# Optimization experiments

Measured on AMD Instinct MI355X. Metric: run time of the kernel, lower is better.

Reference implementation:

```python
import jax, jax.numpy as jnp
import numpy as np

D_MODEL = 1024
N_HEADS = 16
HEAD_DIM = D_MODEL // N_HEADS
NEG = -10000.0  # module uses -10000, not -inf


def setup_inputs() -> dict:
    key = jax.random.key(0)
    ks = jax.random.split(key, 8)
    B, T = 4, 2048
    q = jax.random.normal(ks[0], (B, T, D_MODEL), dtype=jnp.float32)
    k = jax.random.normal(ks[1], (B, T, D_MODEL), dtype=jnp.float32)
    v = jax.random.normal(ks[2], (B, T, D_MODEL), dtype=jnp.float32)
    attn_mask = jnp.ones((B, T), dtype=jnp.float32)
    # xavier_uniform for square [d, d] weights: limit = sqrt(6/(d+d))
    lim = float(np.sqrt(6.0 / (D_MODEL + D_MODEL)))
    Wq = jax.random.uniform(ks[3], (D_MODEL, D_MODEL), jnp.float32, -lim, lim)
    Wk = jax.random.uniform(ks[4], (D_MODEL, D_MODEL), jnp.float32, -lim, lim)
    Wv = jax.random.uniform(ks[5], (D_MODEL, D_MODEL), jnp.float32, -lim, lim)
    Wo = jax.random.uniform(ks[6], (D_MODEL, D_MODEL), jnp.float32, -lim, lim)
    return {"q": q, "k": k, "v": v, "attn_mask": attn_mask,
            "Wq": Wq, "Wk": Wk, "Wv": Wv, "Wo": Wo, "mask_future": 1}


def _split_heads(x):
    B, T, _ = x.shape
    return x.reshape(B, T, N_HEADS, HEAD_DIM).transpose(0, 2, 1, 3)  # [B,H,T,D]


def reference(q, k, v, attn_mask, Wq, Wk, Wv, Wo, mask_future):
    # torch Linear: y = x @ W.T  (weights stored [out, in])
    qh = _split_heads(jnp.einsum('btd,ed->bte', q, Wq))
    kh = _split_heads(jnp.einsum('btd,ed->bte', k, Wk))
    vh = _split_heads(jnp.einsum('btd,ed->bte', v, Wv))
    L, S = qh.shape[-2], kh.shape[-2]
    # dual scale: each of q and k scaled by 1/d**0.25
    scale = 1.0 / jnp.sqrt(jnp.sqrt(jnp.float32(HEAD_DIM)))
    scores = jnp.einsum('bhld,bhsd->bhls', qh * scale, kh * scale)
    if mask_future:
        causal_bias = jnp.triu(jnp.full((L, S), NEG, dtype=scores.dtype), k=1)
        scores = scores + causal_bias
    # padding mask: attn_mask [B, S] -> broadcast [B,1,1,S]; 0 entries -> -10000
    pad = attn_mask[:, None, None, :]
    scores = jnp.where(pad == 0, jnp.asarray(NEG, scores.dtype), scores)
    probs = jax.nn.softmax(scores, axis=-1)  # dropout p=0.0 -> identity
    ctx = jnp.einsum('bhls,bhsd->bhld', probs, vh)
    B = ctx.shape[0]
    ctx = ctx.transpose(0, 2, 1, 3).reshape(B, L, D_MODEL)
    return jnp.einsum('btd,ed->bte', ctx, Wo)
```

## Files before the change

kernel.cpp:

```cpp
#include <hip/hip_runtime.h>

typedef unsigned short u16;
typedef __attribute__((ext_vector_type(8))) _Float16 f16x8;
typedef __attribute__((ext_vector_type(2))) __fp16 fp16v2;
typedef __attribute__((ext_vector_type(4))) float f32x4;
typedef __attribute__((ext_vector_type(16))) float f32x16;

#define T_SEQ 2048
#define NH 16
#define DH 64
#define DM 1024
#define NEG2 (-14426.95f)
#define QS2 (0.42466089f)

__device__ __forceinline__ unsigned pk2(float a, float b) {
  union { fp16v2 v; unsigned u; } c;
  c.v = __builtin_amdgcn_cvt_pkrtz(a, b);
  return c.u;
}
__device__ __forceinline__ u16 f2h(float a) {
  union { _Float16 h; u16 u; } c; c.h = (_Float16)a; return c.u;
}

__device__ __forceinline__ void async_load16(const void* g, void* l) {
  __builtin_amdgcn_global_load_lds(
      (const __attribute__((address_space(1))) unsigned int*)(g),
      (__attribute__((address_space(3))) unsigned int*)(l), 16, 0, 0);
}

__global__ __launch_bounds__(256) void convert_all(
    const float* __restrict__ q, const float* __restrict__ k, const float* __restrict__ v,
    const float* __restrict__ Wq, const float* __restrict__ Wk, const float* __restrict__ Wv,
    const float* __restrict__ Wo, u16* __restrict__ xb, u16* __restrict__ wb) {
  int blk = blockIdx.x;
  const float* src; u16* dst;
  if (blk < 12288) {
    int s = blk >> 12;
    src = (s == 0) ? q : (s == 1) ? k : v;
    dst = xb + (size_t)s * 8388608u;
    blk &= 4095;
  } else {
    int s = (blk - 12288) >> 9;
    src = (s == 0) ? Wq : (s == 1) ? Wk : (s == 2) ? Wv : Wo;
    dst = wb + (size_t)s * 1048576u;
    blk = (blk - 12288) & 511;
  }
  size_t base = (size_t)blk * 2048 + (size_t)threadIdx.x * 8;
  float4 a = *(const float4*)(src + base);
  float4 b2 = *(const float4*)(src + base + 4);
  uint4 st;
  st.x = pk2(a.x, a.y); st.y = pk2(a.z, a.w);
  st.z = pk2(b2.x, b2.y); st.w = pk2(b2.z, b2.w);
  *(uint4*)(dst + base) = st;
}

__global__ __launch_bounds__(256) void gemm_qkv(const u16* __restrict__ A,
                                                const u16* __restrict__ Wqb,
                                                const u16* __restrict__ Wkb,
                                                const u16* __restrict__ Wvb,
                                                u16* __restrict__ Qh, u16* __restrict__ Kh,
                                                u16* __restrict__ VTh) {
  __shared__ char lds[33792];
  const int tid = threadIdx.x;
  const int wid = tid >> 6, lane = tid & 63;
  const int l32 = lane & 31, lh = lane >> 5;
  const int m0 = blockIdx.x * 128;
  const int n0 = blockIdx.y * 128;
  const int which = n0 >> 10;
  const int n0l = n0 & 1023;
  const u16* As = A + (size_t)which * 8388608u;
  const u16* Bw = (which == 0) ? Wqb : (which == 1) ? Wkb : Wvb;
  const int wm = wid >> 1, wn = wid & 1;
  char* const rbase = (which < 2) ? (lds + 16384) : lds;
  char* const cbase = (which < 2) ? lds : (lds + 16384);
  f32x16 acc[2][2] = {};

  for (int kt = 0; kt < 1024; kt += 64) {
    __syncthreads();
    for (int i = 0; i < 4; ++i) {
      int p = wid * 4 + i;
      int mt = p >> 2, ks = p & 3;
      int col = kt + ks * 16 + lh * 8;
      async_load16(As + (size_t)(m0 + mt * 32 + l32) * 1024 + col, lds + p * 1024);
      async_load16(Bw + (size_t)(n0l + mt * 32 + l32) * 1024 + col, lds + 16384 + p * 1024);
    }
    __syncthreads();
    for (int ks = 0; ks < 4; ++ks) {
      f16x8 rf[2], cf[2];
      for (int i = 0; i < 2; ++i) {
        rf[i] = *(const f16x8*)(rbase + ((wm * 2 + i) * 4 + ks) * 1024 + lane * 16);
        cf[i] = *(const f16x8*)(cbase + ((wn * 2 + i) * 4 + ks) * 1024 + lane * 16);
      }
      for (int i = 0; i < 2; ++i)
        for (int j = 0; j < 2; ++j)
          acc[i][j] = __builtin_amdgcn_mfma_f32_32x32x16_f16(rf[i], cf[j], acc[i][j], 0, 0, 0);
    }
  }

  const float s = (which < 2) ? QS2 : 1.0f;
  __syncthreads();
  for (int i = 0; i < 2; ++i)
    for (int j = 0; j < 2; ++j) {
      int colb = wn * 64 + j * 32 + l32;
      int rowb = wm * 64 + i * 32 + 4 * lh;
      for (int g = 0; g < 4; ++g) {
        uint2 pv;
        pv.x = pk2(acc[i][j][4 * g + 0] * s, acc[i][j][4 * g + 1] * s);
        pv.y = pk2(acc[i][j][4 * g + 2] * s, acc[i][j][4 * g + 3] * s);
        *(uint2*)(lds + colb * 264 + (rowb + 8 * g) * 2) = pv;
      }
    }
  __syncthreads();

  const int b = m0 >> 11, t0 = m0 & 2047, h0 = n0l >> 6;
  if (which < 2) {
    u16* O = which ? Kh : Qh;
    for (int p = 0; p < 8; ++p) {
      int row = p * 16 + (tid >> 4);
      int seg = tid & 15;
      uint4 val = *(const uint4*)(lds + row * 264 + seg * 16);
      int hl = seg >> 3, dh0 = (seg & 7) * 8;
      *(uint4*)(O + (((size_t)(b * NH + h0 + hl) * T_SEQ + t0 + row) << 6) + dh0) = val;
    }
  } else {
    for (int p = 0; p < 8; ++p) {
      int row = p * 16 + (tid >> 4);
      int seg = tid & 15;
      uint4 val = *(const uint4*)(lds + row * 264 + seg * 16);
      int h = h0 + (row >> 6), dh = row & 63;
      *(uint4*)(VTh + (((size_t)(b * NH + h) * DH + dh) << 11) + t0 + seg * 8) = val;
    }
  }
}

__global__ __launch_bounds__(256) void gemm_out(const u16* __restrict__ A,
                                                const u16* __restrict__ Bw,
                                                float* __restrict__ O) {
  __shared__ char lds[32768];
  const int tid = threadIdx.x;
  const int wid = tid >> 6, lane = tid & 63;
  const int l32 = lane & 31, lh = lane >> 5;
  const int m0 = blockIdx.x * 128, n0 = blockIdx.y * 128;
  const int wm = wid >> 1, wn = wid & 1;
  f32x16 acc[2][2] = {};

  for (int kt = 0; kt < 1024; kt += 64) {
    __syncthreads();
    for (int i = 0; i < 4; ++i) {
      int p = wid * 4 + i;
      int mt = p >> 2, ks = p & 3;
      int col = kt + ks * 16 + lh * 8;
      async_load16(A + (size_t)(m0 + mt * 32 + l32) * 1024 + col, lds + p * 1024);
      async_load16(Bw + (size_t)(n0 + mt * 32 + l32) * 1024 + col, lds + 16384 + p * 1024);
    }
    __syncthreads();
    for (int ks = 0; ks < 4; ++ks) {
      f16x8 af[2], bf[2];
      for (int i = 0; i < 2; ++i) {
        af[i] = *(const f16x8*)(lds + ((wm * 2 + i) * 4 + ks) * 1024 + lane * 16);
        bf[i] = *(const f16x8*)(lds + 16384 + ((wn * 2 + i) * 4 + ks) * 1024 + lane * 16);
      }
      for (int i = 0; i < 2; ++i)
        for (int j = 0; j < 2; ++j)
          acc[i][j] = __builtin_amdgcn_mfma_f32_32x32x16_f16(af[i], bf[j], acc[i][j], 0, 0, 0);
    }
  }
  for (int i = 0; i < 2; ++i)
    for (int j = 0; j < 2; ++j) {
      int col = n0 + wn * 64 + j * 32 + l32;
      int rowb = m0 + wm * 64 + i * 32 + 4 * lh;
      for (int g = 0; g < 4; ++g)
        for (int rr = 0; rr < 4; ++rr)
          O[(size_t)(rowb + 8 * g + rr) * 1024 + col] = acc[i][j][4 * g + rr];
    }
}

__global__ __launch_bounds__(512) void attn_kernel(const u16* __restrict__ Qh,
                                                   const u16* __restrict__ Kh,
                                                   const u16* __restrict__ VTh,
                                                   const float* __restrict__ attn_mask,
                                                   const int* __restrict__ mfp,
                                                   u16* __restrict__ ctx) {
  __shared__ char kls[8192];
  __shared__ char vls[8192];
  __shared__ char pls[8][2048];
  __shared__ float maskb[T_SEQ];
  __shared__ int mzf;

  const int tid = threadIdx.x;
  const int wid = tid >> 6, lane = tid & 63;
  const int lm = lane & 15, lq = lane >> 4;
  const int bid = blockIdx.x;
  const int bh_i = bid & 63, p8 = bid >> 6;
  const int b = bh_i >> 4, h = bh_i & 15;
  const int mf = *mfp;
  const size_t bh = (size_t)(b * NH + h);
  const u16* Qbh = Qh + bh * T_SEQ * DH;
  const u16* Kbh = Kh + bh * T_SEQ * DH;
  const u16* VTbh = VTh + bh * DH * T_SEQ;

  if (tid == 0) mzf = 0;
  __syncthreads();
  {
    int az = 0;
    for (int i = tid; i < T_SEQ; i += 512) {
      float mv = attn_mask[(size_t)b * T_SEQ + i];
      maskb[i] = (mv == 0.0f) ? NEG2 : 0.0f;
      az |= (mv == 0.0f);
    }
    if (az) mzf = 1;
  }
  __syncthreads();
  const int maskzero = mzf;

  for (int half = 0; half < 2; ++half) {
    const int qt = half ? (15 - p8) : p8;
    const int q0 = qt * 128;
    const int qw = q0 + wid * 16;
    f16x8 qf[2];
    qf[0] = *(const f16x8*)(Qbh + (size_t)(qw + lm) * DH + lq * 8);
    qf[1] = *(const f16x8*)(Qbh + (size_t)(qw + lm) * DH + 32 + lq * 8);

    f32x4 acc[4] = {};
    float mprev = -1e30f, lsum = 0.f;

    const int nch = mf ? (qt + 1) * 2 : 32;
    for (int c = 0; c < nch; ++c) {
      const int s0 = c * 64;
      __syncthreads();
      async_load16(Kbh + (size_t)(s0 + (wid >> 1) * 16 + lm) * DH + (wid & 1) * 32 + lq * 8,
                   kls + wid * 1024);
      async_load16(VTbh + (size_t)((wid >> 1) * 16 + lm) * T_SEQ + s0 + (wid & 1) * 32 + lq * 8,
                   vls + wid * 1024);
      __syncthreads();

      f32x4 sc[4];
      for (int st = 0; st < 4; ++st) {
        f32x4 z = {0.f, 0.f, 0.f, 0.f};
        sc[st] = z;
        for (int kk = 0; kk < 2; ++kk) {
          f16x8 kf = *(const f16x8*)(kls + ((st * 2 + kk) * 64 + lane) * 16);
          sc[st] = __builtin_amdgcn_mfma_f32_16x16x32_f16(kf, qf[kk], sc[st], 0, 0, 0);
        }
      }
      if (maskzero) {
        for (int st = 0; st < 4; ++st) {
          f32x4 mb = *(const f32x4*)(maskb + s0 + st * 16 + lq * 4);
          for (int r = 0; r < 4; ++r) sc[st][r] += mb[r];
        }
      }
      if (mf && (s0 + 64 > qw)) {
        int qg = qw + lm;
        for (int st = 0; st < 4; ++st)
          for (int r = 0; r < 4; ++r)
            if (s0 + st * 16 + lq * 4 + r > qg) sc[st][r] = NEG2;
      }
      float mx = fmaxf(fmaxf(sc[0][0], sc[0][1]), fmaxf(sc[0][2], sc[0][3]));
      for (int st = 1; st < 4; ++st) {
        float t2 = fmaxf(fmaxf(sc[st][0], sc[st][1]), fmaxf(sc[st][2], sc[st][3]));
        mx = fmaxf(mx, t2);
      }
      mx = fmaxf(mx, __shfl_xor(mx, 16));
      mx = fmaxf(mx, __shfl_xor(mx, 32));
      float mn = mprev;
      if (__ballot(mx > mprev) != 0ull) {
        mn = fmaxf(mprev, mx);
        float alpha = exp2f(mprev - mn);
        for (int r = 0; r < 4; ++r) {
          float ar = __shfl(alpha, lq * 4 + r);
          for (int nt = 0; nt < 4; ++nt) acc[nt][r] *= ar;
        }
        lsum *= alpha;
        mprev = mn;
      }
      float ps = 0.f;
      for (int st = 0; st < 4; ++st)
        for (int r = 0; r < 4; ++r) {
          float p = exp2f(sc[st][r] - mn);
          sc[st][r] = p;
          ps += p;
        }
      ps += __shfl_xor(ps, 16);
      ps += __shfl_xor(ps, 32);
      lsum += ps;
      {
        char* pw = pls[wid];
        for (int st = 0; st < 4; ++st) {
          int kk = st >> 1;
          int lqp = (st & 1) * 2 + (lq >> 1);
          uint2 pv;
          pv.x = pk2(sc[st][0], sc[st][1]);
          pv.y = pk2(sc[st][2], sc[st][3]);
          *(uint2*)(pw + kk * 1024 + (lqp * 16 + lm) * 16 + (lq & 1) * 8) = pv;
        }
      }
      asm volatile("s_waitcnt lgkmcnt(0)" ::: "memory");
      for (int kk = 0; kk < 2; ++kk) {
        f16x8 pf = *(const f16x8*)(pls[wid] + kk * 1024 + lane * 16);
        for (int nt = 0; nt < 4; ++nt) {
          f16x8 vf = *(const f16x8*)(vls + ((nt * 2 + kk) * 64 + lane) * 16);
          acc[nt] = __builtin_amdgcn_mfma_f32_16x16x32_f16(pf, vf, acc[nt], 0, 0, 0);
        }
      }
    }
    float inv = 1.0f / lsum;
    for (int r = 0; r < 4; ++r) {
      float ir = __shfl(inv, lq * 4 + r);
      int t = qw + lq * 4 + r;
      for (int nt = 0; nt < 4; ++nt)
        ctx[((size_t)(b * T_SEQ + t) * DM) + h * DH + nt * 16 + lm] = f2h(acc[nt][r] * ir);
    }
  }
}

extern "C" void kernel_launch(void* const* d_in, const int* in_sizes, int n_in,
                              void* d_out, int out_size, void* d_ws, size_t ws_size,
                              hipStream_t stream) {
  const float* q = (const float*)d_in[0];
  const float* k = (const float*)d_in[1];
  const float* v = (const float*)d_in[2];
  const float* attn_mask = (const float*)d_in[3];
  const float* Wq = (const float*)d_in[4];
  const float* Wk = (const float*)d_in[5];
  const float* Wv = (const float*)d_in[6];
  const float* Wo = (const float*)d_in[7];
  const int* mf = (const int*)d_in[8];

  u16* ws = (u16*)d_ws;
  u16* qb  = ws;
  u16* wqb = ws + 3u * 8388608u;
  u16* wkb = wqb + 1048576u;
  u16* wvb = wkb + 1048576u;
  u16* wob = wvb + 1048576u;
  u16* Qh  = wob + 1048576u;
  u16* Kh  = Qh + 8388608u;
  u16* VTh = Kh + 8388608u;
  u16* ctxb = ws;

  convert_all<<<14336, 256, 0, stream>>>(q, k, v, Wq, Wk, Wv, Wo, qb, wqb);

  dim3 gq(64, 24);
  gemm_qkv<<<gq, 256, 0, stream>>>(qb, wqb, wkb, wvb, Qh, Kh, VTh);

  attn_kernel<<<512, 512, 0, stream>>>(Qh, Kh, VTh, attn_mask, mf, ctxb);

  dim3 gg(64, 8);
  gemm_out<<<gg, 256, 0, stream>>>(ctxb, wob, (float*)d_out);
}
```

Measured before the change: 382.3 us.

## Double-buffer LDS tiles in QKV and output GEMMs with prefetch

```diff
diff --git a/kernel.cpp b/kernel.cpp
--- a/kernel.cpp
+++ b/kernel.cpp
@@ -71,25 +71,33 @@
   const u16* As = A + (size_t)which * 8388608u;
   const u16* Bw = (which == 0) ? Wqb : (which == 1) ? Wkb : Wvb;
   const int wm = wid >> 1, wn = wid & 1;
-  char* const rbase = (which < 2) ? (lds + 16384) : lds;
-  char* const cbase = (which < 2) ? lds : (lds + 16384);
   f32x16 acc[2][2] = {};
 
-  for (int kt = 0; kt < 1024; kt += 64) {
+  const u16* gA = As + (size_t)(m0 + wid * 32 + l32) * 1024 + lh * 8;
+  const u16* gB = Bw + (size_t)(n0l + wid * 32 + l32) * 1024 + lh * 8;
+  async_load16(gA, lds + (wid * 2 + 0) * 1024);
+  async_load16(gA + 16, lds + (wid * 2 + 1) * 1024);
+  async_load16(gB, lds + 8192 + (wid * 2 + 0) * 1024);
+  async_load16(gB + 16, lds + 8192 + (wid * 2 + 1) * 1024);
+
+  for (int it = 0; it < 32; ++it) {
     __syncthreads();
-    for (int i = 0; i < 4; ++i) {
-      int p = wid * 4 + i;
-      int mt = p >> 2, ks = p & 3;
-      int col = kt + ks * 16 + lh * 8;
-      async_load16(As + (size_t)(m0 + mt * 32 + l32) * 1024 + col, lds + p * 1024);
-      async_load16(Bw + (size_t)(n0l + mt * 32 + l32) * 1024 + col, lds + 16384 + p * 1024);
-    }
-    __syncthreads();
-    for (int ks = 0; ks < 4; ++ks) {
+    char* cur = lds + (it & 1) * 16384;
+    if (it < 31) {
+      char* nxt = lds + ((it + 1) & 1) * 16384;
+      int kt = (it + 1) * 32;
+      async_load16(gA + kt, nxt + (wid * 2 + 0) * 1024);
+      async_load16(gA + kt + 16, nxt + (wid * 2 + 1) * 1024);
+      async_load16(gB + kt, nxt + 8192 + (wid * 2 + 0) * 1024);
+      async_load16(gB + kt + 16, nxt + 8192 + (wid * 2 + 1) * 1024);
+    }
+    char* const rb = (which < 2) ? (cur + 8192) : cur;
+    char* const cb = (which < 2) ? cur : (cur + 8192);
+    for (int ks = 0; ks < 2; ++ks) {
       f16x8 rf[2], cf[2];
       for (int i = 0; i < 2; ++i) {
-        rf[i] = *(const f16x8*)(rbase + ((wm * 2 + i) * 4 + ks) * 1024 + lane * 16);
-        cf[i] = *(const f16x8*)(cbase + ((wn * 2 + i) * 4 + ks) * 1024 + lane * 16);
+        rf[i] = *(const f16x8*)(rb + ((wm * 2 + i) * 2 + ks) * 1024 + lane * 16);
+        cf[i] = *(const f16x8*)(cb + ((wn * 2 + i) * 2 + ks) * 1024 + lane * 16);
       }
       for (int i = 0; i < 2; ++i)
         for (int j = 0; j < 2; ++j)
@@ -144,21 +152,29 @@
   const int wm = wid >> 1, wn = wid & 1;
   f32x16 acc[2][2] = {};
 
-  for (int kt = 0; kt < 1024; kt += 64) {
+  const u16* gA = A + (size_t)(m0 + wid * 32 + l32) * 1024 + lh * 8;
+  const u16* gB = Bw + (size_t)(n0 + wid * 32 + l32) * 1024 + lh * 8;
+  async_load16(gA, lds + (wid * 2 + 0) * 1024);
+  async_load16(gA + 16, lds + (wid * 2 + 1) * 1024);
+  async_load16(gB, lds + 8192 + (wid * 2 + 0) * 1024);
+  async_load16(gB + 16, lds + 8192 + (wid * 2 + 1) * 1024);
+
+  for (int it = 0; it < 32; ++it) {
     __syncthreads();
-    for (int i = 0; i < 4; ++i) {
-      int p = wid * 4 + i;
-      int mt = p >> 2, ks = p & 3;
-      int col = kt + ks * 16 + lh * 8;
-      async_load16(A + (size_t)(m0 + mt * 32 + l32) * 1024 + col, lds + p * 1024);
-      async_load16(Bw + (size_t)(n0 + mt * 32 + l32) * 1024 + col, lds + 16384 + p * 1024);
-    }
-    __syncthreads();
-    for (int ks = 0; ks < 4; ++ks) {
+    char* cur = lds + (it & 1) * 16384;
+    if (it < 31) {
+      char* nxt = lds + ((it + 1) & 1) * 16384;
+      int kt = (it + 1) * 32;
+      async_load16(gA + kt, nxt + (wid * 2 + 0) * 1024);
+      async_load16(gA + kt + 16, nxt + (wid * 2 + 1) * 1024);
+      async_load16(gB + kt, nxt + 8192 + (wid * 2 + 0) * 1024);
+      async_load16(gB + kt + 16, nxt + 8192 + (wid * 2 + 1) * 1024);
+    }
+    for (int ks = 0; ks < 2; ++ks) {
       f16x8 af[2], bf[2];
       for (int i = 0; i < 2; ++i) {
-        af[i] = *(const f16x8*)(lds + ((wm * 2 + i) * 4 + ks) * 1024 + lane * 16);
-        bf[i] = *(const f16x8*)(lds + 16384 + ((wn * 2 + i) * 4 + ks) * 1024 + lane * 16);
+        af[i] = *(const f16x8*)(cur + ((wm * 2 + i) * 2 + ks) * 1024 + lane * 16);
+        bf[i] = *(const f16x8*)(cur + 8192 + ((wn * 2 + i) * 2 + ks) * 1024 + lane * 16);
       }
       for (int i = 0; i < 2; ++i)
         for (int j = 0; j < 2; ++j)
```

Result: no change. 375.9 us (-1.7%).
